# Performance work log

Measured on AMD Instinct MI355X. Metric: run time of the kernel, lower is better.

The kernel has to match this reference:

```python
import jax, jax.numpy as jnp
import numpy as np

N_NODES = 50000
N_EDGES = 1600000
DIM = 128          # input_dim == hidden_dim == embed_dim
N_LAYERS = 5
NEG_SLOPE = 0.2    # PyG GATv2Conv default


def setup_inputs() -> dict:
    key = jax.random.key(0)
    ks = jax.random.split(key, 8)
    s = 1.0 / np.sqrt(DIM)
    x = jax.random.normal(ks[0], (N_NODES, DIM), dtype=jnp.float32)
    edge_index = jax.random.randint(ks[1], (2, N_EDGES), 0, N_NODES, dtype=jnp.int64)
    # stacked per-layer params (all dims are 128 so layers stack cleanly)
    Wl = jax.random.normal(ks[2], (N_LAYERS, DIM, DIM), dtype=jnp.float32) * s
    bl = jax.random.normal(ks[3], (N_LAYERS, DIM), dtype=jnp.float32) * 0.01
    Wr = jax.random.normal(ks[4], (N_LAYERS, DIM, DIM), dtype=jnp.float32) * s
    br = jax.random.normal(ks[5], (N_LAYERS, DIM), dtype=jnp.float32) * 0.01
    att = jax.random.normal(ks[6], (N_LAYERS, DIM), dtype=jnp.float32) * s
    bias = jax.random.normal(ks[7], (N_LAYERS, DIM), dtype=jnp.float32) * 0.01
    return {"x": x, "edge_index": edge_index, "Wl": Wl, "bl": bl,
            "Wr": Wr, "br": br, "att": att, "bias": bias}


def _gatv2_layer(x, src, dst, Wl, bl, Wr, br, att, bias):
    # x: [N, D]; src/dst: [E'] (self loops already appended)
    n = x.shape[0]
    xl = x @ Wl + bl                      # [N, D]  (source transform; also the message)
    xr = x @ Wr + br                      # [N, D]  (target transform)
    # per-edge GATv2 score: att . LeakyReLU(xl[src] + xr[dst])
    e = jax.nn.leaky_relu(xl[src] + xr[dst], NEG_SLOPE) @ att   # [E']
    # numerically stable segment-softmax over incoming edges of each dst node
    m = jax.ops.segment_max(e, dst, num_segments=n)
    m = jnp.where(jnp.isfinite(m), m, jnp.zeros_like(m))
    p = jnp.exp(e - m[dst])
    z = jax.ops.segment_sum(p, dst, num_segments=n)
    alpha = p / jnp.maximum(z[dst], jnp.asarray(1e-16, p.dtype))  # [E']
    out = jax.ops.segment_sum(alpha[:, None] * xl[src], dst, num_segments=n)
    return out + bias


def reference(x, edge_index, Wl, bl, Wr, br, att, bias):
    n = x.shape[0]
    # PyG GATv2Conv default add_self_loops=True; edges identical across layers -> append once
    loop = jnp.arange(n, dtype=edge_index.dtype)
    src = jnp.concatenate([edge_index[0], loop])
    dst = jnp.concatenate([edge_index[1], loop])
    h = x
    for i in range(N_LAYERS):
        h = _gatv2_layer(h, src, dst, Wl[i], bl[i], Wr[i], br[i], att[i], bias[i])
        if i < N_LAYERS - 1:
            h = jax.nn.relu(h)
    # global_mean_pool with batch=None -> mean over all nodes, shape [1, embed_dim]
    return jnp.mean(h, axis=0, keepdims=True)
```

## Files before the change

kernel.cpp:

```cpp
#include <hip/hip_runtime.h>
#include <hip/hip_bf16.h>

#define N_NODES 50000
#define N_EDGES 1600000
#define DIM 128
#define N_LAYERS 5
#define NEG 0.2f

#define NBKT 196
#define BCAP_A 9472
#define PBLK 196
#define EPB 8192
#define SEGCAP 12288
#define SENT N_NODES
#define LOG2E 1.4426950408889634f

typedef unsigned short u16;
typedef unsigned char u8;
typedef unsigned int u32;
using short8 = __attribute__((ext_vector_type(8))) short;
using f32x4  = __attribute__((ext_vector_type(4))) float;
typedef float f32x2 __attribute__((ext_vector_type(2)));

union FragU { uint4 u; short8 s; };

__device__ __forceinline__ f32x2 bf2v(u32 u) {
    union { u32 i; float f; } lo, hi;
    lo.i = u << 16;
    hi.i = u & 0xffff0000u;
    f32x2 r; r.x = lo.f; r.y = hi.f;
    return r;
}
__device__ __forceinline__ u16 f2bf(float f) {
    union { float f; u32 u; } v; v.f = f;
    u32 r = v.u + 0x7fffu + ((v.u >> 16) & 1u);
    return (u16)(r >> 16);
}
__device__ __forceinline__ u32 cvtpk(float a, float b) {
    u32 r;
    asm("v_cvt_pk_bf16_f32 %0, %1, %2" : "=v"(r) : "v"(a), "v"(b));
    return r;
}
__device__ __forceinline__ int clampi(int v) {
    v = (v < 0) ? 0 : v;
    return (v >= N_NODES) ? (N_NODES - 1) : v;
}
template<int CTRL>
__device__ __forceinline__ float rradd(float v) {
    int t = __builtin_amdgcn_update_dpp(0, __float_as_int(v), CTRL, 0xF, 0xF, true);
    return v + __int_as_float(t);
}

__global__ void k_probe(const int* __restrict__ ei32, int* __restrict__ flags,
                        int* __restrict__ bcnt) {
    __shared__ int cnt;
    int t = threadIdx.x;
    if (t == 0) cnt = 0;
    __syncthreads();
    if (ei32[2 * t + 1] == 0) atomicAdd(&cnt, 1);
    if (t < NBKT) bcnt[t] = 0;
    __syncthreads();
    if (t == 0) flags[0] = (cnt >= 255) ? 1 : 0;
}

__device__ __forceinline__ int ldidx(const void* ei, long long i, int m64) {
    int v = m64 ? (int)(((const long long*)ei)[i]) : ((const int*)ei)[i];
    return clampi(v);
}

__global__ void k_cvt_x(const float* __restrict__ x, u16* __restrict__ xb) {
    int i = blockIdx.x * 256 + threadIdx.x;
    float2 v = *(const float2*)(x + (size_t)i * 2);
    ((u32*)xb)[i] = cvtpk(v.x, v.y);
}

__global__ void k_cvt_w(const float* __restrict__ Wl, const float* __restrict__ Wr,
                        uint4* __restrict__ Wtg) {
    int id = blockIdx.x * 256 + threadIdx.x;
    if (id >= N_LAYERS * 16 * 256) return;
    int l = id >> 12;
    int rem = id & 4095;
    int kc = rem >> 8;
    int n = rem & 255;
    const float* W = (n < 128) ? (Wl + (size_t)l * DIM * DIM + n)
                               : (Wr + (size_t)l * DIM * DIM + (n - 128));
    u16 c[8];
#pragma unroll
    for (int j = 0; j < 8; ++j) c[j] = f2bf(W[(size_t)(kc * 8 + j) * DIM]);
    uint4 o;
    o.x = (u32)c[0] | ((u32)c[1] << 16);
    o.y = (u32)c[2] | ((u32)c[3] << 16);
    o.z = (u32)c[4] | ((u32)c[5] << 16);
    o.w = (u32)c[6] | ((u32)c[7] << 16);
    Wtg[(size_t)l * 4096 + n * 16 + (kc ^ (n & 15))] = o;
}

__global__ __launch_bounds__(1024) void k_part(
    const void* __restrict__ ei, const int* __restrict__ flags,
    int* __restrict__ bcnt, u32* __restrict__ bpk)
{
    __shared__ u32 ebuf[EPB];
    __shared__ u8  bkb[EPB];
    __shared__ int lh[NBKT];
    __shared__ int lb[NBKT + 1];
    __shared__ int gst[NBKT];
    __shared__ int sc[256];

    const int tid = threadIdx.x;
    const int m64 = flags[0];
    const long long e0 = (long long)blockIdx.x * EPB;

    for (int i = tid; i < NBKT; i += 1024) lh[i] = 0;
    __syncthreads();

    u32 pay[8];
    u32 meta[8];
    int nv = 0;
#pragma unroll
    for (int i = 0; i < 8; ++i) {
        long long e = e0 + i * 1024 + tid;
        if (e < N_EDGES) {
            int s = ldidx(ei, e, m64);
            int d = ldidx(ei, (long long)N_EDGES + e, m64);
            int b = d >> 8;
            int rank = atomicAdd(&lh[b], 1);
            pay[i] = (u32)s | ((u32)(d & 255) << 16);
            meta[i] = (u32)b | ((u32)rank << 8);
            nv = i + 1;
        }
    }
    __syncthreads();

    if (tid < 256) sc[tid] = (tid < NBKT) ? lh[tid] : 0;
    __syncthreads();
    for (int off = 1; off < 256; off <<= 1) {
        int v = 0;
        if (tid < 256 && tid >= off) v = sc[tid - off];
        __syncthreads();
        if (tid < 256) sc[tid] += v;
        __syncthreads();
    }
    if (tid < NBKT) lb[tid] = sc[tid] - lh[tid];
    if (tid == 0) lb[NBKT] = 0;
    if (tid < NBKT) gst[tid] = atomicAdd(&bcnt[tid], lh[tid]);
    __syncthreads();

#pragma unroll
    for (int i = 0; i < 8; ++i) {
        if (i < nv) {
            int b = (int)(meta[i] & 255);
            int rank = (int)(meta[i] >> 8);
            int p = lb[b] + rank;
            ebuf[p] = pay[i];
            bkb[p] = (u8)b;
        }
    }
    __syncthreads();

    int total = (e0 + EPB <= N_EDGES) ? EPB : (int)(N_EDGES - e0);
    for (int i = tid; i < total; i += 1024) {
        int b = (int)bkb[i];
        int off = gst[b] + (i - lb[b]);
        if (off < BCAP_A)
            bpk[(size_t)b * BCAP_A + off] = ebuf[i];
    }
}

__global__ __launch_bounds__(256) void k_deg(
    const u32* __restrict__ bpk, const int* __restrict__ bcnt,
    const void* __restrict__ ei, const int* __restrict__ flags,
    int* __restrict__ row_off, int* __restrict__ btot)
{
    __shared__ int dh[256];
    __shared__ int sc[256];
    int b = blockIdx.x;
    int tid = threadIdx.x;
    dh[tid] = 0;
    __syncthreads();
    int cnt = bcnt[b];
    if (cnt <= BCAP_A) {
        for (int i = tid; i < cnt; i += 256)
            atomicAdd(&dh[(bpk[(size_t)b * BCAP_A + i] >> 16) & 255], 1);
    } else {
        int m64 = flags[0];
        for (long long e = tid; e < N_EDGES; e += 256) {
            int d = ldidx(ei, (long long)N_EDGES + e, m64);
            if ((d >> 8) == b) atomicAdd(&dh[d & 255], 1);
        }
    }
    __syncthreads();
    int d = b * 256 + tid;
    int v = 0;
    if (d < N_NODES) {
        v = (dh[tid] + 1 + 3) & ~3;
        if (v < 16) v = 16;
    }
    sc[tid] = v;
    __syncthreads();
    for (int off = 1; off < 256; off <<= 1) {
        int t = (tid >= off) ? sc[tid - off] : 0;
        __syncthreads();
        sc[tid] += t;
        __syncthreads();
    }
    if (d < N_NODES) row_off[d] = sc[tid] - v;
    if (tid == 255) btot[b] = sc[255];
}

__global__ void k_bscan(const int* __restrict__ btot, int* __restrict__ boff,
                        int* __restrict__ row_off) {
    __shared__ int sc[256];
    int tid = threadIdx.x;
    int v = (tid < NBKT) ? btot[tid] : 0;
    sc[tid] = v;
    __syncthreads();
    for (int off = 1; off < 256; off <<= 1) {
        int t = (tid >= off) ? sc[tid - off] : 0;
        __syncthreads();
        sc[tid] += t;
        __syncthreads();
    }
    if (tid < NBKT) boff[tid] = sc[tid] - v;
    if (tid == NBKT - 1) row_off[N_NODES] = sc[tid];
}

__global__ __launch_bounds__(256) void k_scat(
    const u32* __restrict__ bpk, const int* __restrict__ bcnt,
    int* __restrict__ row_off, const int* __restrict__ boff,
    const int* __restrict__ btot, u32* __restrict__ col,
    const void* __restrict__ ei, const int* __restrict__ flags)
{
    __shared__ u32 stage[SEGCAP];
    __shared__ int cur[256];
    int b = blockIdx.x;
    int tid = threadIdx.x;
    int d_lo = b * 256;
    int d_hi = d_lo + 256; if (d_hi > N_NODES) d_hi = N_NODES;
    int base0 = boff[b];
    int seglen = btot[b];
    if (seglen > SEGCAP) seglen = SEGCAP;

    int d = d_lo + tid;
    int rloc = 0;
    int ext = 0;
    if (d < d_hi) {
        rloc = row_off[d];
        ext = (d + 1 < d_hi) ? row_off[d + 1] : btot[b];
        if (ext > SEGCAP) ext = SEGCAP;
        if (rloc < SEGCAP) stage[rloc] = (u32)d * 256u;
        cur[tid] = rloc + 1;
    }
    __syncthreads();

    int cnt = bcnt[b];
    if (cnt <= BCAP_A) {
        for (int i = tid; i < cnt; i += 256) {
            u32 p = bpk[(size_t)b * BCAP_A + i];
            int pos = atomicAdd(&cur[(p >> 16) & 255], 1);
            if (pos < SEGCAP) stage[pos] = (p & 0xffffu) * 256u;
        }
    } else {
        int m64 = flags[0];
        for (long long e = tid; e < N_EDGES; e += 256) {
            int dd = ldidx(ei, (long long)N_EDGES + e, m64);
            if ((dd >> 8) == b) {
                int s = ldidx(ei, e, m64);
                int pos = atomicAdd(&cur[dd & 255], 1);
                if (pos < SEGCAP) stage[pos] = (u32)s * 256u;
            }
        }
    }
    __syncthreads();
    if (d < d_hi) {
        for (int i = cur[tid]; i < ext; ++i) stage[i] = (u32)SENT * 256u;
    }
    __syncthreads();
    for (int i = tid; i < seglen; i += 256)
        col[base0 + i] = stage[i];
    if (d < d_hi) row_off[d] = base0 + rloc;
}

__global__ __launch_bounds__(256) void k_mm(
    const u16* __restrict__ hb,
    const uint4* __restrict__ Wtg,
    const float* __restrict__ bl, const float* __restrict__ br,
    const float* __restrict__ att,
    u16* __restrict__ xlb,
    u16* __restrict__ xrb)
{
    __shared__ uint4 wsh[4096];
    const int tid = threadIdx.x;
#pragma unroll
    for (int i = 0; i < 16; ++i) wsh[tid + i * 256] = Wtg[tid + i * 256];

    const int wave = tid >> 6, lane = tid & 63;
    const int q = lane >> 4, nn = lane & 15;
    const int mA0 = blockIdx.x * 128 + wave * 16 + nn;
    const int mA1 = mA0 + 64;

    FragU a0[4], a1[4];
    const uint4 az = make_uint4(0, 0, 0, 0);
#pragma unroll
    for (int s = 0; s < 4; ++s) {
        a0[s].u = (mA0 < N_NODES)
                ? *(const uint4*)(hb + (size_t)mA0 * DIM + s * 32 + q * 8) : az;
        a1[s].u = (mA1 < N_NODES)
                ? *(const uint4*)(hb + (size_t)mA1 * DIM + s * 32 + q * 8) : az;
    }
    __syncthreads();

    f32x4 acc0[16], acc1[16];
#pragma unroll
    for (int i = 0; i < 16; ++i) {
        acc0[i] = (f32x4){0.f, 0.f, 0.f, 0.f};
        acc1[i] = (f32x4){0.f, 0.f, 0.f, 0.f};
    }

#pragma unroll
    for (int s = 0; s < 4; ++s) {
#pragma unroll
        for (int nt = 0; nt < 16; ++nt) {
            int n = nt * 16 + nn;
            int kc = s * 4 + q;
            FragU b;
            b.u = wsh[n * 16 + (kc ^ (n & 15))];
            acc0[nt] = __builtin_amdgcn_mfma_f32_16x16x32_bf16(b.s, a0[s].s, acc0[nt], 0, 0, 0);
            acc1[nt] = __builtin_amdgcn_mfma_f32_16x16x32_bf16(b.s, a1[s].s, acc1[nt], 0, 0, 0);
        }
    }

    const bool v0 = (mA0 < N_NODES);
    const bool v1 = (mA1 < N_NODES);
#pragma unroll
    for (int nt = 0; nt < 16; ++nt) {
        int n0 = nt * 16 + q * 4;
        bool isL = (n0 < 128);
        const float* bp = isL ? (bl + n0) : (br + (n0 - 128));
        float4 bv = *(const float4*)bp;
        uint2 o0, o1;
        o0.x = cvtpk(acc0[nt][0] + bv.x, acc0[nt][1] + bv.y);
        o0.y = cvtpk(acc0[nt][2] + bv.z, acc0[nt][3] + bv.w);
        o1.x = cvtpk(acc1[nt][0] + bv.x, acc1[nt][1] + bv.y);
        o1.y = cvtpk(acc1[nt][2] + bv.z, acc1[nt][3] + bv.w);
        int nc = isL ? n0 : (n0 - 128);
        if (v0) {
            u16* dst = (isL ? xlb : xrb) + (size_t)mA0 * DIM + nc;
            *(uint2*)dst = o0;
        }
        if (v1) {
            u16* dst = (isL ? xlb : xrb) + (size_t)mA1 * DIM + nc;
            *(uint2*)dst = o1;
        }
    }

    if (blockIdx.x == 0 && tid < DIM) {
        float s = att[tid];
        xlb[(size_t)SENT * DIM + tid] = f2bf(s >= 0.f ? -10000.f : 10000.f);
    }
}

#define PROC(U) do {                                                          \
    f32x2 x01 = bf2v((U).x), x23 = bf2v((U).y);                               \
    f32x2 x45 = bf2v((U).z), x67 = bf2v((U).w);                               \
    f32x2 z01 = x01 + xr01, z23 = x23 + xr23;                                 \
    f32x2 z45 = x45 + xr45, z67 = x67 + xr67;                                 \
    z01 = __builtin_elementwise_max(z01, z01 * negv);                         \
    z23 = __builtin_elementwise_max(z23, z23 * negv);                         \
    z45 = __builtin_elementwise_max(z45, z45 * negv);                         \
    z67 = __builtin_elementwise_max(z67, z67 * negv);                         \
    f32x2 pp2 = at01 * z01;                                                   \
    pp2 = at23 * z23 + pp2;                                                   \
    pp2 = at45 * z45 + pp2;                                                   \
    pp2 = at67 * z67 + pp2;                                                   \
    float pp = pp2.x + pp2.y;                                                 \
    pp = rradd<0x121>(pp);                                                    \
    pp = rradd<0x122>(pp);                                                    \
    pp = rradd<0x124>(pp);                                                    \
    pp = rradd<0x128>(pp);                                                    \
    float w_ = __builtin_amdgcn_exp2f(pp);                                    \
    lsum += w_;                                                               \
    f32x2 wv; wv.x = w_; wv.y = w_;                                           \
    ac01 = wv * x01 + ac01; ac23 = wv * x23 + ac23;                           \
    ac45 = wv * x45 + ac45; ac67 = wv * x67 + ac67;                           \
} while (0)

#define LDQ(U, Q) do {                                                        \
    u32 ob_ = __shfl(off, ((Q) << 2) + g, 64);                                \
    (U) = *(const uint4*)(xbp + (size_t)(ob_ + dofs));                        \
} while (0)

template <int RELU>
__global__ __launch_bounds__(64) void k_edge(
    const u16* __restrict__ xlb, const u16* __restrict__ xrb,
    const int* __restrict__ row_off, const u32* __restrict__ col,
    const float* __restrict__ att, const float* __restrict__ bias,
    u16* __restrict__ hout)
{
    const int node = blockIdx.x;
    const int lane = threadIdx.x & 63;
    const int g = lane >> 4;
    const int t = lane & 15;

    const int d0 = t * 8;
    const u32 dofs = (u32)(t << 4);
    const char* xbp = (const char*)xlb;

    uint4 xru = *(const uint4*)(xrb + (size_t)node * DIM + d0);
    f32x2 xr01 = bf2v(xru.x), xr23 = bf2v(xru.y), xr45 = bf2v(xru.z), xr67 = bf2v(xru.w);
    float2 a0 = *(const float2*)(att + d0);
    float2 a1 = *(const float2*)(att + d0 + 2);
    float2 a2 = *(const float2*)(att + d0 + 4);
    float2 a3 = *(const float2*)(att + d0 + 6);
    f32x2 at01, at23, at45, at67;
    at01.x = a0.x * LOG2E; at01.y = a0.y * LOG2E;
    at23.x = a1.x * LOG2E; at23.y = a1.y * LOG2E;
    at45.x = a2.x * LOG2E; at45.y = a2.y * LOG2E;
    at67.x = a3.x * LOG2E; at67.y = a3.y * LOG2E;
    f32x2 negv; negv.x = NEG; negv.y = NEG;

    const int beg = __builtin_amdgcn_readfirstlane(row_off[node]);
    const int end = __builtin_amdgcn_readfirstlane(row_off[node + 1]);
    const int n = end - beg;
    const int nreg = (n < 64) ? n : 64;
    const int nq = nreg >> 2;

    u32 off = col[beg + lane];

    f32x2 ac01, ac23, ac45, ac67;
    ac01.x = ac01.y = ac23.x = ac23.y = 0.f;
    ac45.x = ac45.y = ac67.x = ac67.y = 0.f;
    float lsum = 0.f;

    uint4 u0, u1, u2, u3;
    LDQ(u0, 0); LDQ(u1, 1); LDQ(u2, 2); LDQ(u3, 3);

    int q = 0;
    for (; q + 8 <= nq; q += 4) {
        PROC(u0); LDQ(u0, q + 4);
        PROC(u1); LDQ(u1, q + 5);
        PROC(u2); LDQ(u2, q + 6);
        PROC(u3); LDQ(u3, q + 7);
    }
    PROC(u0); if (q + 4 < nq) LDQ(u0, q + 4);
    PROC(u1); if (q + 5 < nq) LDQ(u1, q + 5);
    PROC(u2); if (q + 6 < nq) LDQ(u2, q + 6);
    PROC(u3); if (q + 7 < nq) LDQ(u3, q + 7);
    q += 4;
    if (q     < nq) PROC(u0);
    if (q + 1 < nq) PROC(u1);
    if (q + 2 < nq) PROC(u2);

    for (int j = beg + 64 + g; j < end; j += 4) {
        u32 ob_ = col[j];
        uint4 u = *(const uint4*)(xbp + (size_t)(ob_ + dofs));
        PROC(u);
    }

    float accv[8] = {ac01.x, ac01.y, ac23.x, ac23.y, ac45.x, ac45.y, ac67.x, ac67.y};
#pragma unroll
    for (int i = 0; i < 8; ++i) {
        accv[i] += __shfl_xor(accv[i], 16, 64);
        accv[i] += __shfl_xor(accv[i], 32, 64);
    }
    lsum += __shfl_xor(lsum, 16, 64);
    lsum += __shfl_xor(lsum, 32, 64);

    if (g == 0) {
        float inv = 1.f / fmaxf(lsum, 1e-16f);
        float4 b0 = *(const float4*)(bias + d0);
        float4 b1 = *(const float4*)(bias + d0 + 4);
        float o0 = accv[0] * inv + b0.x;
        float o1 = accv[1] * inv + b0.y;
        float o2 = accv[2] * inv + b0.z;
        float o3 = accv[3] * inv + b0.w;
        float o4 = accv[4] * inv + b1.x;
        float o5 = accv[5] * inv + b1.y;
        float o6 = accv[6] * inv + b1.z;
        float o7 = accv[7] * inv + b1.w;
        if (RELU) {
            o0 = fmaxf(o0, 0.f); o1 = fmaxf(o1, 0.f);
            o2 = fmaxf(o2, 0.f); o3 = fmaxf(o3, 0.f);
            o4 = fmaxf(o4, 0.f); o5 = fmaxf(o5, 0.f);
            o6 = fmaxf(o6, 0.f); o7 = fmaxf(o7, 0.f);
        }
        uint4 o;
        o.x = cvtpk(o0, o1);
        o.y = cvtpk(o2, o3);
        o.z = cvtpk(o4, o5);
        o.w = cvtpk(o6, o7);
        *(uint4*)(hout + (size_t)node * DIM + d0) = o;
    }
}

__global__ __launch_bounds__(256) void k_mean_part(const u16* __restrict__ hb,
                                                   float* __restrict__ part) {
    __shared__ float sh[4][16][8];
    int t = threadIdx.x;
    int b = blockIdx.x;
    int c0 = (t & 15) * 8;
    int rl = t >> 4;
    int n0 = b * 400;
    float acc[8] = {0.f, 0.f, 0.f, 0.f, 0.f, 0.f, 0.f, 0.f};
    for (int i = 0; i < 25; ++i) {
        int r = n0 + rl + i * 16;
        uint4 v = *(const uint4*)(hb + (size_t)r * DIM + c0);
        f32x2 p0 = bf2v(v.x), p1 = bf2v(v.y), p2 = bf2v(v.z), p3 = bf2v(v.w);
        acc[0] += p0.x; acc[1] += p0.y;
        acc[2] += p1.x; acc[3] += p1.y;
        acc[4] += p2.x; acc[5] += p2.y;
        acc[6] += p3.x; acc[7] += p3.y;
    }
#pragma unroll
    for (int i = 0; i < 8; ++i) {
        acc[i] += __shfl_xor(acc[i], 16, 64);
        acc[i] += __shfl_xor(acc[i], 32, 64);
    }
    int wave = t >> 6;
    if ((t & 63) < 16) {
#pragma unroll
        for (int i = 0; i < 8; ++i) sh[wave][t & 15][i] = acc[i];
    }
    __syncthreads();
    if (t < 16) {
#pragma unroll
        for (int i = 0; i < 8; ++i) {
            float s = sh[0][t][i] + sh[1][t][i] + sh[2][t][i] + sh[3][t][i];
            part[b * DIM + t * 8 + i] = s;
        }
    }
}

__global__ void k_mean_final(const float* __restrict__ part, float* __restrict__ out) {
    int d = threadIdx.x;
    float s = 0.f;
    for (int b = 0; b < 125; ++b) s += part[b * DIM + d];
    out[d] = s * (1.f / (float)N_NODES);
}

extern "C" void kernel_launch(void* const* d_in, const int* in_sizes, int n_in,
                              void* d_out, int out_size, void* d_ws, size_t ws_size,
                              hipStream_t stream) {
    int ix, iei, iWl, ibl, iWr, ibr, iatt, ibias;
    if (in_sizes[0] == N_NODES * DIM) {
        ix = 0; iei = 1; iWl = 2; ibl = 3; iWr = 4; ibr = 5; iatt = 6; ibias = 7;
    } else {
        iWl = 0; iWr = 1; iatt = 2; ibias = 3; ibl = 4; ibr = 5; iei = 6; ix = 7;
    }
    const float* x    = (const float*)d_in[ix];
    const void*  ei   = d_in[iei];
    const float* Wl   = (const float*)d_in[iWl];
    const float* bl   = (const float*)d_in[ibl];
    const float* Wr   = (const float*)d_in[iWr];
    const float* br   = (const float*)d_in[ibr];
    const float* att  = (const float*)d_in[iatt];
    const float* bias = (const float*)d_in[ibias];
    float* out = (float*)d_out;

    char* w = (char*)d_ws;
    float* part = (float*)w;      w += (size_t)256 * DIM * 4;
    uint4* Wtg = (uint4*)w;       w += (size_t)N_LAYERS * 4096 * 16;
    u16* xb  = (u16*)w;           w += (size_t)N_NODES * DIM * 2;
    u16* hb  = (u16*)w;           w += (size_t)N_NODES * DIM * 2;
    u16* xlb = (u16*)w;           w += (size_t)(N_NODES + 1) * DIM * 2;
    u16* xrb = (u16*)w;           w += (size_t)N_NODES * DIM * 2;
    int* row_off = (int*)w;       w += (size_t)(N_NODES + 4) * 4;
    int* flags = (int*)w;         w += 64;
    int* bcnt = (int*)w;          w += (size_t)(NBKT + 4) * 4;
    int* btot = (int*)w;          w += (size_t)(NBKT + 4) * 4;
    int* boff = (int*)w;          w += (size_t)(NBKT + 4) * 4;
    u32* bpk = (u32*)w;           w += (size_t)NBKT * BCAP_A * 4;
    u32* col = (u32*)w;           w += (size_t)(N_EDGES + 8 * N_NODES + 64) * 4;

    k_probe<<<1, 256, 0, stream>>>((const int*)ei, flags, bcnt);
    k_cvt_x<<<(N_NODES * DIM / 2 + 255) / 256, 256, 0, stream>>>(x, xb);
    k_cvt_w<<<(N_LAYERS * 4096 + 255) / 256, 256, 0, stream>>>(Wl, Wr, Wtg);
    k_part<<<PBLK, 1024, 0, stream>>>(ei, flags, bcnt, bpk);
    k_deg<<<NBKT, 256, 0, stream>>>(bpk, bcnt, ei, flags, row_off, btot);
    k_bscan<<<1, 256, 0, stream>>>(btot, boff, row_off);
    k_scat<<<NBKT, 256, 0, stream>>>(bpk, bcnt, row_off, boff, btot, col, ei, flags);

    const int mm_grid = (N_NODES + 127) / 128;

    for (int layer = 0; layer < N_LAYERS; ++layer) {
        const uint4* Wp = Wtg + (size_t)layer * 4096;
        const float* blp = bl + (size_t)layer * DIM;
        const float* brp = br + (size_t)layer * DIM;
        const float* ap  = att + (size_t)layer * DIM;
        const float* bp  = bias + (size_t)layer * DIM;

        const u16* hin = (layer == 0) ? xb : hb;
        k_mm<<<mm_grid, 256, 0, stream>>>(hin, Wp, blp, brp, ap, xlb, xrb);

        if (layer < N_LAYERS - 1)
            k_edge<1><<<N_NODES, 64, 0, stream>>>(xlb, xrb, row_off, col, ap, bp, hb);
        else
            k_edge<0><<<N_NODES, 64, 0, stream>>>(xlb, xrb, row_off, col, ap, bp, hb);
    }

    k_mean_part<<<125, 256, 0, stream>>>(hb, part);
    k_mean_final<<<1, 128, 0, stream>>>(part, out);
}
```

Before: 485.7 us.

## Fold probe and bucket-scan kernels into neighbors and make GEMM persistent

Merges the edge-dtype probe into the weight-conversion kernel and replaces the separate bucket scan with a per-block prefix reduction inside the scatter kernel, removing two small kernel launches. The per-layer GEMM is changed to a fixed 256-block grid-stride loop, so each block loads the weight tile into shared memory once and reuses it across up to two node tiles. This removes launch overhead and repeated weight loads, at the cost of redundant prefix reductions per scatter block and lower parallelism in the GEMM.

```diff
diff --git a/kernel.cpp b/kernel.cpp
--- a/kernel.cpp
+++ b/kernel.cpp
@@ -51,18 +51,6 @@
     return v + __int_as_float(t);
 }
 
-__global__ void k_probe(const int* __restrict__ ei32, int* __restrict__ flags,
-                        int* __restrict__ bcnt) {
-    __shared__ int cnt;
-    int t = threadIdx.x;
-    if (t == 0) cnt = 0;
-    __syncthreads();
-    if (ei32[2 * t + 1] == 0) atomicAdd(&cnt, 1);
-    if (t < NBKT) bcnt[t] = 0;
-    __syncthreads();
-    if (t == 0) flags[0] = (cnt >= 255) ? 1 : 0;
-}
-
 __device__ __forceinline__ int ldidx(const void* ei, long long i, int m64) {
     int v = m64 ? (int)(((const long long*)ei)[i]) : ((const int*)ei)[i];
     return clampi(v);
@@ -75,7 +63,19 @@
 }
 
 __global__ void k_cvt_w(const float* __restrict__ Wl, const float* __restrict__ Wr,
-                        uint4* __restrict__ Wtg) {
+                        uint4* __restrict__ Wtg,
+                        const int* __restrict__ ei32, int* __restrict__ flags,
+                        int* __restrict__ bcnt) {
+    __shared__ int cnt;
+    if (blockIdx.x == 0) {
+        int t = threadIdx.x;
+        if (t == 0) cnt = 0;
+        __syncthreads();
+        if (ei32[2 * t + 1] == 0) atomicAdd(&cnt, 1);
+        if (t < NBKT) bcnt[t] = 0;
+        __syncthreads();
+        if (t == 0) flags[0] = (cnt >= 255) ? 1 : 0;
+    }
     int id = blockIdx.x * 256 + threadIdx.x;
     if (id >= N_LAYERS * 16 * 256) return;
     int l = id >> 12;
@@ -207,36 +207,28 @@
     if (tid == 255) btot[b] = sc[255];
 }
 
-__global__ void k_bscan(const int* __restrict__ btot, int* __restrict__ boff,
-                        int* __restrict__ row_off) {
-    __shared__ int sc[256];
-    int tid = threadIdx.x;
-    int v = (tid < NBKT) ? btot[tid] : 0;
-    sc[tid] = v;
-    __syncthreads();
-    for (int off = 1; off < 256; off <<= 1) {
-        int t = (tid >= off) ? sc[tid - off] : 0;
-        __syncthreads();
-        sc[tid] += t;
-        __syncthreads();
-    }
-    if (tid < NBKT) boff[tid] = sc[tid] - v;
-    if (tid == NBKT - 1) row_off[N_NODES] = sc[tid];
-}
-
 __global__ __launch_bounds__(256) void k_scat(
     const u32* __restrict__ bpk, const int* __restrict__ bcnt,
-    int* __restrict__ row_off, const int* __restrict__ boff,
-    const int* __restrict__ btot, u32* __restrict__ col,
+    int* __restrict__ row_off, const int* __restrict__ btot,
+    u32* __restrict__ col,
     const void* __restrict__ ei, const int* __restrict__ flags)
 {
     __shared__ u32 stage[SEGCAP];
     __shared__ int cur[256];
+    __shared__ int red[256];
     int b = blockIdx.x;
     int tid = threadIdx.x;
+
+    red[tid] = (tid < b) ? btot[tid] : 0;
+    __syncthreads();
+    for (int off = 128; off > 0; off >>= 1) {
+        if (tid < off) red[tid] += red[tid + off];
+        __syncthreads();
+    }
+    int base0 = red[0];
+
     int d_lo = b * 256;
     int d_hi = d_lo + 256; if (d_hi > N_NODES) d_hi = N_NODES;
-    int base0 = boff[b];
     int seglen = btot[b];
     if (seglen > SEGCAP) seglen = SEGCAP;
 
@@ -278,6 +270,7 @@
     for (int i = tid; i < seglen; i += 256)
         col[base0 + i] = stage[i];
     if (d < d_hi) row_off[d] = base0 + rloc;
+    if (b == NBKT - 1 && tid == 0) row_off[N_NODES] = base0 + btot[b];
 }
 
 __global__ __launch_bounds__(256) void k_mm(
@@ -292,64 +285,67 @@
     const int tid = threadIdx.x;
 #pragma unroll
     for (int i = 0; i < 16; ++i) wsh[tid + i * 256] = Wtg[tid + i * 256];
+    __syncthreads();
 
     const int wave = tid >> 6, lane = tid & 63;
     const int q = lane >> 4, nn = lane & 15;
-    const int mA0 = blockIdx.x * 128 + wave * 16 + nn;
-    const int mA1 = mA0 + 64;
-
-    FragU a0[4], a1[4];
-    const uint4 az = make_uint4(0, 0, 0, 0);
-#pragma unroll
-    for (int s = 0; s < 4; ++s) {
-        a0[s].u = (mA0 < N_NODES)
-                ? *(const uint4*)(hb + (size_t)mA0 * DIM + s * 32 + q * 8) : az;
-        a1[s].u = (mA1 < N_NODES)
-                ? *(const uint4*)(hb + (size_t)mA1 * DIM + s * 32 + q * 8) : az;
-    }
-    __syncthreads();
-
-    f32x4 acc0[16], acc1[16];
-#pragma unroll
-    for (int i = 0; i < 16; ++i) {
-        acc0[i] = (f32x4){0.f, 0.f, 0.f, 0.f};
-        acc1[i] = (f32x4){0.f, 0.f, 0.f, 0.f};
-    }
-
-#pragma unroll
-    for (int s = 0; s < 4; ++s) {
+
+    for (int tile = blockIdx.x; tile * 128 < N_NODES; tile += 256) {
+        const int mA0 = tile * 128 + wave * 16 + nn;
+        const int mA1 = mA0 + 64;
+
+        FragU a0[4], a1[4];
+        const uint4 az = make_uint4(0, 0, 0, 0);
+#pragma unroll
+        for (int s = 0; s < 4; ++s) {
+            a0[s].u = (mA0 < N_NODES)
+                    ? *(const uint4*)(hb + (size_t)mA0 * DIM + s * 32 + q * 8) : az;
+            a1[s].u = (mA1 < N_NODES)
+                    ? *(const uint4*)(hb + (size_t)mA1 * DIM + s * 32 + q * 8) : az;
+        }
+
+        f32x4 acc0[16], acc1[16];
+#pragma unroll
+        for (int i = 0; i < 16; ++i) {
+            acc0[i] = (f32x4){0.f, 0.f, 0.f, 0.f};
+            acc1[i] = (f32x4){0.f, 0.f, 0.f, 0.f};
+        }
+
+#pragma unroll
+        for (int s = 0; s < 4; ++s) {
+#pragma unroll
+            for (int nt = 0; nt < 16; ++nt) {
+                int n = nt * 16 + nn;
+                int kc = s * 4 + q;
+                FragU b;
+                b.u = wsh[n * 16 + (kc ^ (n & 15))];
+                acc0[nt] = __builtin_amdgcn_mfma_f32_16x16x32_bf16(b.s, a0[s].s, acc0[nt], 0, 0, 0);
+                acc1[nt] = __builtin_amdgcn_mfma_f32_16x16x32_bf16(b.s, a1[s].s, acc1[nt], 0, 0, 0);
+            }
+        }
+
+        const bool v0 = (mA0 < N_NODES);
+        const bool v1 = (mA1 < N_NODES);
 #pragma unroll
         for (int nt = 0; nt < 16; ++nt) {
-            int n = nt * 16 + nn;
-            int kc = s * 4 + q;
-            FragU b;
-            b.u = wsh[n * 16 + (kc ^ (n & 15))];
-            acc0[nt] = __builtin_amdgcn_mfma_f32_16x16x32_bf16(b.s, a0[s].s, acc0[nt], 0, 0, 0);
-            acc1[nt] = __builtin_amdgcn_mfma_f32_16x16x32_bf16(b.s, a1[s].s, acc1[nt], 0, 0, 0);
-        }
-    }
-
-    const bool v0 = (mA0 < N_NODES);
-    const bool v1 = (mA1 < N_NODES);
-#pragma unroll
-    for (int nt = 0; nt < 16; ++nt) {
-        int n0 = nt * 16 + q * 4;
-        bool isL = (n0 < 128);
-        const float* bp = isL ? (bl + n0) : (br + (n0 - 128));
-        float4 bv = *(const float4*)bp;
-        uint2 o0, o1;
-        o0.x = cvtpk(acc0[nt][0] + bv.x, acc0[nt][1] + bv.y);
-        o0.y = cvtpk(acc0[nt][2] + bv.z, acc0[nt][3] + bv.w);
-        o1.x = cvtpk(acc1[nt][0] + bv.x, acc1[nt][1] + bv.y);
-        o1.y = cvtpk(acc1[nt][2] + bv.z, acc1[nt][3] + bv.w);
-        int nc = isL ? n0 : (n0 - 128);
-        if (v0) {
-            u16* dst = (isL ? xlb : xrb) + (size_t)mA0 * DIM + nc;
-            *(uint2*)dst = o0;
-        }
-        if (v1) {
-            u16* dst = (isL ? xlb : xrb) + (size_t)mA1 * DIM + nc;
-            *(uint2*)dst = o1;
+            int n0 = nt * 16 + q * 4;
+            bool isL = (n0 < 128);
+            const float* bp = isL ? (bl + n0) : (br + (n0 - 128));
+            float4 bv = *(const float4*)bp;
+            uint2 o0, o1;
+            o0.x = cvtpk(acc0[nt][0] + bv.x, acc0[nt][1] + bv.y);
+            o0.y = cvtpk(acc0[nt][2] + bv.z, acc0[nt][3] + bv.w);
+            o1.x = cvtpk(acc1[nt][0] + bv.x, acc1[nt][1] + bv.y);
+            o1.y = cvtpk(acc1[nt][2] + bv.z, acc1[nt][3] + bv.w);
+            int nc = isL ? n0 : (n0 - 128);
+            if (v0) {
+                u16* dst = (isL ? xlb : xrb) + (size_t)mA0 * DIM + nc;
+                *(uint2*)dst = o0;
+            }
+            if (v1) {
+                u16* dst = (isL ? xlb : xrb) + (size_t)mA1 * DIM + nc;
+                *(uint2*)dst = o1;
+            }
         }
     }
 
@@ -567,19 +563,15 @@
     int* flags = (int*)w;         w += 64;
     int* bcnt = (int*)w;          w += (size_t)(NBKT + 4) * 4;
     int* btot = (int*)w;          w += (size_t)(NBKT + 4) * 4;
-    int* boff = (int*)w;          w += (size_t)(NBKT + 4) * 4;
     u32* bpk = (u32*)w;           w += (size_t)NBKT * BCAP_A * 4;
     u32* col = (u32*)w;           w += (size_t)(N_EDGES + 8 * N_NODES + 64) * 4;
 
-    k_probe<<<1, 256, 0, stream>>>((const int*)ei, flags, bcnt);
     k_cvt_x<<<(N_NODES * DIM / 2 + 255) / 256, 256, 0, stream>>>(x, xb);
-    k_cvt_w<<<(N_LAYERS * 4096 + 255) / 256, 256, 0, stream>>>(Wl, Wr, Wtg);
+    k_cvt_w<<<(N_LAYERS * 4096 + 255) / 256, 256, 0, stream>>>(Wl, Wr, Wtg,
+                                                               (const int*)ei, flags, bcnt);
     k_part<<<PBLK, 1024, 0, stream>>>(ei, flags, bcnt, bpk);
     k_deg<<<NBKT, 256, 0, stream>>>(bpk, bcnt, ei, flags, row_off, btot);
-    k_bscan<<<1, 256, 0, stream>>>(btot, boff, row_off);
-    k_scat<<<NBKT, 256, 0, stream>>>(bpk, bcnt, row_off, boff, btot, col, ei, flags);
-
-    const int mm_grid = (N_NODES + 127) / 128;
+    k_scat<<<NBKT, 256, 0, stream>>>(bpk, bcnt, row_off, btot, col, ei, flags);
 
     for (int layer = 0; layer < N_LAYERS; ++layer) {
         const uint4* Wp = Wtg + (size_t)layer * 4096;
@@ -589,7 +581,7 @@
         const float* bp  = bias + (size_t)layer * DIM;
 
         const u16* hin = (layer == 0) ? xb : hb;
-        k_mm<<<mm_grid, 256, 0, stream>>>(hin, Wp, blp, brp, ap, xlb, xrb);
+        k_mm<<<256, 256, 0, stream>>>(hin, Wp, blp, brp, ap, xlb, xrb);
 
         if (layer < N_LAYERS - 1)
             k_edge<1><<<N_NODES, 64, 0, stream>>>(xlb, xrb, row_off, col, ap, bp, hb);
```

Result: no change. 494.4 us (+1.8%).
